# Optimization experiments

Hardware: AMD Instinct MI355X
Metric: run time of the kernel (lower is better)

Reference implementation:

```python
import jax, jax.numpy as jnp
import numpy as np

N, L, S, E, D = 8, 2048, 2048, 1024, 64

def setup_inputs() -> dict:
    key = jax.random.key(0)
    ks = jax.random.split(key, 6)
    q = jax.random.normal(ks[0], (N, L, E), dtype=jnp.float32)
    k = jax.random.normal(ks[1], (N, S, E), dtype=jnp.float32)
    v = jax.random.normal(ks[2], (N, S, E), dtype=jnp.float32)
    # Linear weights stored as [E, D] so projection is x @ W
    Wq = jax.random.normal(ks[3], (E, D), dtype=jnp.float32) / np.sqrt(E)
    Wk = jax.random.normal(ks[4], (E, D), dtype=jnp.float32) / np.sqrt(E)
    Wv = jax.random.normal(ks[5], (E, D), dtype=jnp.float32) / np.sqrt(E)
    # causal bool mask: True above diagonal => masked to -inf
    attn_mask = jnp.triu(jnp.ones((L, S), dtype=bool), k=1)
    return {"q": q, "k": k, "v": v, "Wq": Wq, "Wk": Wk, "Wv": Wv, "attn_mask": attn_mask}


def reference(q, k, v, Wq, Wk, Wv, attn_mask):
    qh = q @ Wq                      # [N, L, D]
    kh = k @ Wk                      # [N, S, D]
    vh = v @ Wv                      # [N, S, D]
    # NOTE: source divides by d**(-1/2), i.e. multiplies by sqrt(D) (faithful bug)
    scale = jnp.asarray(D, dtype=qh.dtype) ** 0.5
    scores = jnp.einsum("nld,nsd->nls", qh, kh) * scale   # [N, L, S]
    scores = jnp.where(attn_mask[None, :, :], -jnp.inf, scores)
    weights = jax.nn.softmax(scores, axis=-1)
    out = jnp.einsum("nls,nsd->nld", weights, vh)          # [N, L, D]
    return out
```

## Files before the change

### kernel.cpp

```cpp
#include <hip/hip_runtime.h>
#include <math.h>

#define NB 8
#define LQ 2048
#define LOG2E 1.44269504088896f

typedef __attribute__((ext_vector_type(4))) float f32x4;
typedef __attribute__((ext_vector_type(8))) short s16x8;

__device__ __forceinline__ unsigned f2bf_u(float f) {
  unsigned u = __builtin_bit_cast(unsigned, f);
  u += 0x7FFFu + ((u >> 16) & 1u);
  return u >> 16;
}
__device__ __forceinline__ float bf2f(unsigned h) {
  unsigned u = h << 16;
  return __builtin_bit_cast(float, u);
}

#define MFMA16 __builtin_amdgcn_mfma_f32_16x16x32_bf16

__global__ __launch_bounds__(256) void wsplit_kernel(
    const float* __restrict__ Wq, const float* __restrict__ Wk,
    const float* __restrict__ Wv, short* __restrict__ wt) {
  int bk = blockIdx.x;
  int z = blockIdx.y;
  const float* W = (z == 0) ? Wq : (z == 1) ? Wk : Wv;
  __shared__ float tile[64][65];
  int t = threadIdx.x;
#pragma unroll
  for (int it = 0; it < 16; ++it) {
    int kk = it * 4 + (t >> 6);
    int d = t & 63;
    tile[kk][d] = W[(size_t)(bk * 64 + kk) * 64 + d];
  }
  __syncthreads();
#pragma unroll
  for (int it = 0; it < 16; ++it) {
    int d = it * 4 + (t >> 6);
    int kk = t & 63;
    float f = tile[kk][d];
    unsigned h = f2bf_u(f);
    unsigned l = f2bf_u(f - bf2f(h));
    wt[((size_t)(z * 2 + 0) * 64 + d) * 1024 + bk * 64 + kk] = (short)h;
    wt[((size_t)(z * 2 + 1) * 64 + d) * 1024 + bk * 64 + kk] = (short)l;
  }
}

__global__ __launch_bounds__(256, 3) void proj_kernel(
    const float* __restrict__ xq, const float* __restrict__ xk,
    const float* __restrict__ xv, const short* __restrict__ wt,
    short* __restrict__ qhi, short* __restrict__ qlo,
    short* __restrict__ khi, short* __restrict__ klo,
    short* __restrict__ vhT) {
  int z = blockIdx.y;
  const float* x = (z == 0) ? xq : (z == 1) ? xk : xv;
  const short* wthi = wt + (size_t)(z * 2 + 0) * 64 * 1024;
  const short* wtlo = wt + (size_t)(z * 2 + 1) * 64 * 1024;
  int row0 = blockIdx.x * 64;
  int t = threadIdx.x;
  int wv = t >> 6, lane = t & 63;
  int c = lane & 15, quad = lane >> 4;
  const float* xp = x + (size_t)(row0 + wv * 16 + c) * 1024 + quad * 8;
  f32x4 acc[4] = {};
  f32x4 p0 = *(const f32x4*)(xp + 0);
  f32x4 p1 = *(const f32x4*)(xp + 4);
  f32x4 p2 = *(const f32x4*)(xp + 32);
  f32x4 p3 = *(const f32x4*)(xp + 36);
  for (int kb = 0; kb < 16; ++kb) {
    s16x8 bh0[4], bl0[4], bh1[4], bl1[4];
    int ko = kb * 64 + quad * 8;
#pragma unroll
    for (int cs = 0; cs < 4; ++cs) {
      const short* bp = wthi + (size_t)(cs * 16 + c) * 1024 + ko;
      const short* lp = wtlo + (size_t)(cs * 16 + c) * 1024 + ko;
      bh0[cs] = *(const s16x8*)(bp);
      bh1[cs] = *(const s16x8*)(bp + 32);
      bl0[cs] = *(const s16x8*)(lp);
      bl1[cs] = *(const s16x8*)(lp + 32);
    }
    s16x8 ah0, al0, ah1, al1;
#pragma unroll
    for (int j = 0; j < 4; ++j) {
      unsigned h;
      h = f2bf_u(p0[j]); ah0[j] = (short)h;     al0[j] = (short)f2bf_u(p0[j] - bf2f(h));
      h = f2bf_u(p1[j]); ah0[4 + j] = (short)h; al0[4 + j] = (short)f2bf_u(p1[j] - bf2f(h));
      h = f2bf_u(p2[j]); ah1[j] = (short)h;     al1[j] = (short)f2bf_u(p2[j] - bf2f(h));
      h = f2bf_u(p3[j]); ah1[4 + j] = (short)h; al1[4 + j] = (short)f2bf_u(p3[j] - bf2f(h));
    }
    if (kb < 15) {
      xp += 64;
      p0 = *(const f32x4*)(xp + 0);
      p1 = *(const f32x4*)(xp + 4);
      p2 = *(const f32x4*)(xp + 32);
      p3 = *(const f32x4*)(xp + 36);
    }
#pragma unroll
    for (int cs = 0; cs < 4; ++cs) {
      acc[cs] = MFMA16(ah0, bh0[cs], acc[cs], 0, 0, 0);
      acc[cs] = MFMA16(ah0, bl0[cs], acc[cs], 0, 0, 0);
      acc[cs] = MFMA16(al0, bh0[cs], acc[cs], 0, 0, 0);
    }
#pragma unroll
    for (int cs = 0; cs < 4; ++cs) {
      acc[cs] = MFMA16(ah1, bh1[cs], acc[cs], 0, 0, 0);
      acc[cs] = MFMA16(ah1, bl1[cs], acc[cs], 0, 0, 0);
      acc[cs] = MFMA16(al1, bh1[cs], acc[cs], 0, 0, 0);
    }
  }
  if (z < 2) {
    short* hi = (z == 0) ? qhi : khi;
    short* lo = (z == 0) ? qlo : klo;
#pragma unroll
    for (int cs = 0; cs < 4; ++cs)
#pragma unroll
      for (int r = 0; r < 4; ++r) {
        int row = row0 + wv * 16 + quad * 4 + r;
        int col = cs * 16 + c;
        float val = acc[cs][r];
        unsigned h = f2bf_u(val);
        unsigned l = f2bf_u(val - bf2f(h));
        hi[(size_t)row * 64 + col] = (short)h;
        lo[(size_t)row * 64 + col] = (short)l;
      }
  } else {
    __shared__ short vtile[64][72];
#pragma unroll
    for (int cs = 0; cs < 4; ++cs)
#pragma unroll
      for (int r = 0; r < 4; ++r)
        vtile[cs * 16 + c][wv * 16 + quad * 4 + r] = (short)f2bf_u(acc[cs][r]);
    __syncthreads();
    int n = row0 >> 11;
    int sbase = row0 & 2047;
    int d = t >> 2, sc = (t & 3) * 16;
#pragma unroll
    for (int j = 0; j < 2; ++j) {
      s16x8 vv = *(const s16x8*)&vtile[d][sc + j * 8];
      *(s16x8*)&vhT[((size_t)n * 64 + d) * LQ + sbase + sc + j * 8] = vv;
    }
  }
}

__global__ __launch_bounds__(256, 3) void attn_kernel(
    const short* __restrict__ qhi, const short* __restrict__ qlo,
    const short* __restrict__ khi, const short* __restrict__ klo,
    const short* __restrict__ vhT, float* __restrict__ outp) {
  int bid = blockIdx.x;
  int n = bid & 7;
  int qt = 127 - (bid >> 3);
  int t = threadIdx.x;
  int wv = t >> 6, lane = t & 63;
  int c = lane & 15, quad = lane >> 4;
  int qr0 = qt * 16;
  __shared__ short pS[4][16][72];
  __shared__ float mS[4][16], lS[4][16];
  __shared__ float oS[4][16][64];
  s16x8 qfh[2], qfl[2];
  size_t qbase = ((size_t)n * LQ + qr0 + c) * 64;
#pragma unroll
  for (int kc = 0; kc < 2; ++kc) {
    qfh[kc] = *(const s16x8*)&qhi[qbase + kc * 32 + quad * 8];
    qfl[kc] = *(const s16x8*)&qlo[qbase + kc * 32 + quad * 8];
  }
  f32x4 o[4] = {};
  float m_r[4], l_r[4];
#pragma unroll
  for (int r = 0; r < 4; ++r) { m_r[r] = -INFINITY; l_r[r] = 0.0f; }
  int ktmax = qt >> 2;
  for (int kt = wv; kt <= ktmax; kt += 4) {
    int s0 = kt * 64;
    size_t kbase = ((size_t)n * LQ + s0) * 64;
    f32x4 sa[4] = {};
#pragma unroll
    for (int ct = 0; ct < 4; ++ct) {
      size_t rb = kbase + (size_t)(ct * 16 + c) * 64;
#pragma unroll
      for (int kc = 0; kc < 2; ++kc) {
        s16x8 bh = *(const s16x8*)&khi[rb + kc * 32 + quad * 8];
        s16x8 bl = *(const s16x8*)&klo[rb + kc * 32 + quad * 8];
        sa[ct] = MFMA16(qfh[kc], bh, sa[ct], 0, 0, 0);
        sa[ct] = MFMA16(qfh[kc], bl, sa[ct], 0, 0, 0);
        sa[ct] = MFMA16(qfl[kc], bh, sa[ct], 0, 0, 0);
      }
    }
    s16x8 vb[4][2];
#pragma unroll
    for (int dt = 0; dt < 4; ++dt)
#pragma unroll
      for (int kc2 = 0; kc2 < 2; ++kc2)
        vb[dt][kc2] = *(const s16x8*)&vhT[((size_t)n * 64 + dt * 16 + c) * LQ +
                                          s0 + kc2 * 32 + quad * 8];
    float sv[4][4];
    bool diag = (kt == ktmax);
#pragma unroll
    for (int ct = 0; ct < 4; ++ct)
#pragma unroll
      for (int r = 0; r < 4; ++r) {
        float xsc = sa[ct][r] * 8.0f;
        if (diag) {
          int sg = s0 + ct * 16 + c;
          int qg = qr0 + quad * 4 + r;
          if (sg > qg) xsc = -INFINITY;
        }
        sv[ct][r] = xsc;
      }
    float alpha[4];
#pragma unroll
    for (int r = 0; r < 4; ++r) {
      float mx = fmaxf(fmaxf(sv[0][r], sv[1][r]), fmaxf(sv[2][r], sv[3][r]));
#pragma unroll
      for (int off = 1; off < 16; off <<= 1) mx = fmaxf(mx, __shfl_xor(mx, off, 64));
      float mnew = fmaxf(m_r[r], mx);
      alpha[r] = exp2f((m_r[r] - mnew) * LOG2E);
      m_r[r] = mnew;
      float rs = 0.0f;
#pragma unroll
      for (int ct = 0; ct < 4; ++ct) {
        float p = exp2f((sv[ct][r] - mnew) * LOG2E);
        sv[ct][r] = p;
        rs += p;
      }
#pragma unroll
      for (int off = 1; off < 16; off <<= 1) rs += __shfl_xor(rs, off, 64);
      l_r[r] = l_r[r] * alpha[r] + rs;
    }
#pragma unroll
    for (int dt = 0; dt < 4; ++dt)
#pragma unroll
      for (int r = 0; r < 4; ++r) o[dt][r] *= alpha[r];
#pragma unroll
    for (int ct = 0; ct < 4; ++ct)
#pragma unroll
      for (int r = 0; r < 4; ++r)
        pS[wv][quad * 4 + r][ct * 16 + c] = (short)f2bf_u(sv[ct][r]);
    s16x8 pa[2];
#pragma unroll
    for (int kc2 = 0; kc2 < 2; ++kc2)
      pa[kc2] = *(const s16x8*)&pS[wv][c][kc2 * 32 + quad * 8];
#pragma unroll
    for (int dt = 0; dt < 4; ++dt)
#pragma unroll
      for (int kc2 = 0; kc2 < 2; ++kc2)
        o[dt] = MFMA16(pa[kc2], vb[dt][kc2], o[dt], 0, 0, 0);
  }
#pragma unroll
  for (int dt = 0; dt < 4; ++dt)
#pragma unroll
    for (int r = 0; r < 4; ++r)
      oS[wv][quad * 4 + r][dt * 16 + c] = o[dt][r];
  if (c == 0) {
#pragma unroll
    for (int r = 0; r < 4; ++r) {
      mS[wv][quad * 4 + r] = m_r[r];
      lS[wv][quad * 4 + r] = l_r[r];
    }
  }
  __syncthreads();
  {
    int r = t >> 4;
    int c4 = (t & 15) * 4;
    float m0 = mS[0][r], m1 = mS[1][r], m2 = mS[2][r], m3 = mS[3][r];
    float mstar = fmaxf(fmaxf(m0, m1), fmaxf(m2, m3));
    float s0 = exp2f((m0 - mstar) * LOG2E);
    float s1 = exp2f((m1 - mstar) * LOG2E);
    float s2 = exp2f((m2 - mstar) * LOG2E);
    float s3 = exp2f((m3 - mstar) * LOG2E);
    float lstar = s0 * lS[0][r] + s1 * lS[1][r] + s2 * lS[2][r] + s3 * lS[3][r];
    float inv = 1.0f / lstar;
    f32x4 oa;
#pragma unroll
    for (int j = 0; j < 4; ++j)
      oa[j] = (s0 * oS[0][r][c4 + j] + s1 * oS[1][r][c4 + j] +
               s2 * oS[2][r][c4 + j] + s3 * oS[3][r][c4 + j]) * inv;
    *(f32x4*)&outp[((size_t)n * LQ + qr0 + r) * 64 + c4] = oa;
  }
}

extern "C" void kernel_launch(void* const* d_in, const int* in_sizes, int n_in,
                              void* d_out, int out_size, void* d_ws, size_t ws_size,
                              hipStream_t stream) {
  const float* q = (const float*)d_in[0];
  const float* k = (const float*)d_in[1];
  const float* v = (const float*)d_in[2];
  const float* Wq = (const float*)d_in[3];
  const float* Wk = (const float*)d_in[4];
  const float* Wv = (const float*)d_in[5];
  float* out = (float*)d_out;

  char* ws = (char*)d_ws;
  short* wt  = (short*)ws;
  short* qhi = (short*)(ws + 786432);
  short* qlo = qhi + (size_t)16384 * 64;
  short* khi = qlo + (size_t)16384 * 64;
  short* klo = khi + (size_t)16384 * 64;
  short* vhT = klo + (size_t)16384 * 64;

  wsplit_kernel<<<dim3(16, 3), 256, 0, stream>>>(Wq, Wk, Wv, wt);
  proj_kernel<<<dim3(256, 3), 256, 0, stream>>>(q, k, v, wt, qhi, qlo, khi, klo, vhT);
  attn_kernel<<<dim3(1024), 256, 0, stream>>>(qhi, qlo, khi, klo, vhT, out);
}
```

Baseline: 327.1 us.

## Stage projection input tiles into LDS via async global_load_lds double buffer

The projection kernel no longer loads x rows straight into registers with strided per-lane loads. It now streams 64x64 fp32 tiles into a double-buffered, XOR-swizzled LDS buffer using global_load_lds, and each wave reads its A fragments back from LDS. The aim is coalesced global reads and overlap of the next tile's load with the current MFMA work. In exchange it uses 32KB more LDS per block, which can lower occupancy under launch_bounds(256,3), and it adds a __syncthreads per k-step.

```diff
diff --git a/kernel.cpp b/kernel.cpp
--- a/kernel.cpp
+++ b/kernel.cpp
@@ -61,53 +61,68 @@
   int t = threadIdx.x;
   int wv = t >> 6, lane = t & 63;
   int c = lane & 15, quad = lane >> 4;
-  const float* xp = x + (size_t)(row0 + wv * 16 + c) * 1024 + quad * 8;
+
+  __shared__ float xa[2][64 * 64];
+  __shared__ short vtile[64][72];
+
+  const float* xg = x + (size_t)row0 * 1024;
+
+#define STAGE(buf, kb)                                                        \
+  {                                                                           \
+    _Pragma("unroll") for (int j = 0; j < 4; ++j) {                           \
+      int row = wv * 16 + j * 4 + quad;                                       \
+      const float* src = xg + (size_t)row * 1024 + (kb) * 64 +                \
+                         ((c ^ (row & 7)) << 2);                              \
+      float* dst = &xa[buf][(wv * 4 + j) * 256];       \
+      __builtin_amdgcn_global_load_lds(                                       \
+          (const __attribute__((address_space(1))) unsigned*)src,             \
+          (__attribute__((address_space(3))) unsigned*)dst, 16, 0, 0);        \
+    }                                                                         \
+  }
+
   f32x4 acc[4] = {};
-  f32x4 p0 = *(const f32x4*)(xp + 0);
-  f32x4 p1 = *(const f32x4*)(xp + 4);
-  f32x4 p2 = *(const f32x4*)(xp + 32);
-  f32x4 p3 = *(const f32x4*)(xp + 36);
+  STAGE(0, 0);
+  __syncthreads();
+  int cur = 0;
+  int rowl = wv * 16 + c;
   for (int kb = 0; kb < 16; ++kb) {
-    s16x8 bh0[4], bl0[4], bh1[4], bl1[4];
+    if (kb < 15) STAGE(cur ^ 1, kb + 1);
+    s16x8 bh[4][2], bl[4][2];
     int ko = kb * 64 + quad * 8;
 #pragma unroll
     for (int cs = 0; cs < 4; ++cs) {
       const short* bp = wthi + (size_t)(cs * 16 + c) * 1024 + ko;
       const short* lp = wtlo + (size_t)(cs * 16 + c) * 1024 + ko;
-      bh0[cs] = *(const s16x8*)(bp);
-      bh1[cs] = *(const s16x8*)(bp + 32);
-      bl0[cs] = *(const s16x8*)(lp);
-      bl1[cs] = *(const s16x8*)(lp + 32);
-    }
-    s16x8 ah0, al0, ah1, al1;
-#pragma unroll
-    for (int j = 0; j < 4; ++j) {
-      unsigned h;
-      h = f2bf_u(p0[j]); ah0[j] = (short)h;     al0[j] = (short)f2bf_u(p0[j] - bf2f(h));
-      h = f2bf_u(p1[j]); ah0[4 + j] = (short)h; al0[4 + j] = (short)f2bf_u(p1[j] - bf2f(h));
-      h = f2bf_u(p2[j]); ah1[j] = (short)h;     al1[j] = (short)f2bf_u(p2[j] - bf2f(h));
-      h = f2bf_u(p3[j]); ah1[4 + j] = (short)h; al1[4 + j] = (short)f2bf_u(p3[j] - bf2f(h));
-    }
-    if (kb < 15) {
-      xp += 64;
-      p0 = *(const f32x4*)(xp + 0);
-      p1 = *(const f32x4*)(xp + 4);
-      p2 = *(const f32x4*)(xp + 32);
-      p3 = *(const f32x4*)(xp + 36);
-    }
-#pragma unroll
-    for (int cs = 0; cs < 4; ++cs) {
-      acc[cs] = MFMA16(ah0, bh0[cs], acc[cs], 0, 0, 0);
-      acc[cs] = MFMA16(ah0, bl0[cs], acc[cs], 0, 0, 0);
-      acc[cs] = MFMA16(al0, bh0[cs], acc[cs], 0, 0, 0);
-    }
-#pragma unroll
-    for (int cs = 0; cs < 4; ++cs) {
-      acc[cs] = MFMA16(ah1, bh1[cs], acc[cs], 0, 0, 0);
-      acc[cs] = MFMA16(ah1, bl1[cs], acc[cs], 0, 0, 0);
-      acc[cs] = MFMA16(al1, bh1[cs], acc[cs], 0, 0, 0);
-    }
-  }
+      bh[cs][0] = *(const s16x8*)(bp);
+      bh[cs][1] = *(const s16x8*)(bp + 32);
+      bl[cs][0] = *(const s16x8*)(lp);
+      bl[cs][1] = *(const s16x8*)(lp + 32);
+    }
+    const float* arow = &xa[cur][rowl * 64];
+#pragma unroll
+    for (int kc = 0; kc < 2; ++kc) {
+      int ch0 = ((kc * 8 + quad * 2 + 0) ^ (c & 7)) << 2;
+      int ch1 = ((kc * 8 + quad * 2 + 1) ^ (c & 7)) << 2;
+      f32x4 a0 = *(const f32x4*)(arow + ch0);
+      f32x4 a1 = *(const f32x4*)(arow + ch1);
+      s16x8 ah, al;
+#pragma unroll
+      for (int j = 0; j < 4; ++j) {
+        unsigned h;
+        h = f2bf_u(a0[j]); ah[j] = (short)h;     al[j] = (short)f2bf_u(a0[j] - bf2f(h));
+        h = f2bf_u(a1[j]); ah[4 + j] = (short)h; al[4 + j] = (short)f2bf_u(a1[j] - bf2f(h));
+      }
+#pragma unroll
+      for (int cs = 0; cs < 4; ++cs) {
+        acc[cs] = MFMA16(ah, bh[cs][kc], acc[cs], 0, 0, 0);
+        acc[cs] = MFMA16(ah, bl[cs][kc], acc[cs], 0, 0, 0);
+        acc[cs] = MFMA16(al, bh[cs][kc], acc[cs], 0, 0, 0);
+      }
+    }
+    __syncthreads();
+    cur ^= 1;
+  }
+#undef STAGE
   if (z < 2) {
     short* hi = (z == 0) ? qhi : khi;
     short* lo = (z == 0) ? qlo : klo;
@@ -124,7 +139,6 @@
         lo[(size_t)row * 64 + col] = (short)l;
       }
   } else {
-    __shared__ short vtile[64][72];
 #pragma unroll
     for (int cs = 0; cs < 4; ++cs)
 #pragma unroll
```

After: 310.3 us. 1.05x faster.
